# Optimization experiments

Measured on AMD Instinct MI355X. Metric: run time of the kernel, lower is better.

Reference implementation:

```python
import jax, jax.numpy as jnp
import numpy as np

N = 100000
E = 640000
D_IN = 128
D_OUT = 128


def setup_inputs() -> dict:
    key = jax.random.key(0)
    k1, k2, k3, k4, k5 = jax.random.split(key, 5)
    x = jax.random.normal(k1, (N, D_IN), dtype=jnp.float32)
    edge_index = jax.random.randint(k2, (2, E), 0, N, dtype=jnp.int64)
    edge_weight = jax.random.uniform(k3, (E,), dtype=jnp.float32)
    W_rel = jax.random.normal(k4, (D_OUT, D_IN), dtype=jnp.float32) / np.sqrt(D_IN)
    W_root = jax.random.normal(k5, (D_OUT, D_IN), dtype=jnp.float32) / np.sqrt(D_IN)
    b = jnp.zeros((D_OUT,), dtype=jnp.float32)
    return {"x": x, "edge_index": edge_index, "edge_weight": edge_weight,
            "W_rel": W_rel, "W_root": W_root, "b": b}


def reference(x, edge_index, edge_weight, W_rel, W_root, b):
    # PyG GraphConv: out_i = W_rel @ (sum_{j -> i} w_ij * x_j) + W_root @ x_i + b
    src = edge_index[0]  # message source (x_j)
    dst = edge_index[1]  # aggregation target
    msg = x[src] * edge_weight[:, None]          # [E, D_IN] gather + scale
    agg = jax.ops.segment_sum(msg, dst, num_segments=x.shape[0])  # [N, D_IN]
    out = agg @ W_rel.T + x @ W_root.T + b       # [N, D_OUT]
    return out
```

## Files before the change

kernel.cpp:

```cpp
#include <hip/hip_runtime.h>
#include <hip/hip_fp16.h>

#define NN 100000
#define EE 640000
#define D 128
#define NBINS NN
#define SCAN_NBLK 98

#define WS_CNT      0
#define WS_OFFS     100000
#define WS_BSUM     200000
#define WS_SW       200192
#define WS_WF       1480192
#define WS_XH       1496576
#define WS_INTS_TOP 7896576

#define WS_WCONV    1480192
#define WS_INTS_MID 1512960

#define PREP_XB 3125
#define PREP_WB 128
#define PREP_HB 2500

typedef __attribute__((ext_vector_type(8))) short    short8v;
typedef __attribute__((ext_vector_type(8))) _Float16 half8v;
typedef __attribute__((ext_vector_type(4))) float    floatx4;
struct __align__(8) half4t { __half2 a, b; };

__device__ inline void split_bf16(float f, short& h, short& l) {
    unsigned u  = __float_as_uint(f);
    unsigned hb = u & 0xFFFF0000u;
    h = (short)(u >> 16);
    float fl = f - __uint_as_float(hb);
    l = (short)(__float_as_uint(fl) >> 16);
}

__global__ __launch_bounds__(256) void scatter_kernel(
    const float* __restrict__ x, const int* __restrict__ ei,
    const float* __restrict__ ew, float* agg)
{
    int gid = blockIdx.x * 256 + threadIdx.x;
    int e = gid >> 7, f = gid & 127;
    if (e >= EE) return;
    float v = x[ei[e] * D + f] * ew[e];
    unsafeAtomicAdd(&agg[ei[EE + e] * D + f], v);
}

__global__ __launch_bounds__(256) void zero_cnt_kernel(int* __restrict__ cnt)
{
    int i = blockIdx.x * 256 + threadIdx.x;
    if (i < NBINS) cnt[i] = 0;
}

__global__ __launch_bounds__(256) void prep_kernel(
    const float* __restrict__ x, const float* __restrict__ Wrel,
    const float* __restrict__ Wroot, const int* __restrict__ ei,
    short* __restrict__ xh, short* __restrict__ Wf, int* __restrict__ cnt)
{
    const int b = blockIdx.x;
    if (b < PREP_XB) {
        const int base = b * 4096 + threadIdx.x * 4;
        float4 v[4];
        #pragma unroll
        for (int u = 0; u < 4; u++)
            v[u] = *(const float4*)&x[base + u * 1024];
        #pragma unroll
        for (int u = 0; u < 4; u++) {
            short4 h;
            h.x = (short)__half_as_ushort(__float2half(v[u].x));
            h.y = (short)__half_as_ushort(__float2half(v[u].y));
            h.z = (short)__half_as_ushort(__float2half(v[u].z));
            h.w = (short)__half_as_ushort(__float2half(v[u].w));
            *(short4*)&xh[base + u * 1024] = h;
        }
    } else if (b < PREP_XB + PREP_WB) {
        int i = (b - PREP_XB) * 256 + threadIdx.x;
        int c = i >> 8, k = i & 255;
        float f = (k < 128) ? Wrel[c * 128 + k] : Wroot[c * 128 + (k - 128)];
        Wf[i] = (short)__half_as_ushort(__float2half(f));
    } else {
        int e = (b - PREP_XB - PREP_WB) * 256 + threadIdx.x;
        if (e < EE) atomicAdd(&cnt[ei[EE + e]], 1);
    }
}

__global__ __launch_bounds__(256) void hist_kernel(
    const int* __restrict__ ei, int* __restrict__ cnt)
{
    int e = blockIdx.x * 256 + threadIdx.x;
    if (e < EE) atomicAdd(&cnt[ei[EE + e]], 1);
}

__global__ __launch_bounds__(256) void wconv_kernel(
    const float* __restrict__ Wrel, const float* __restrict__ Wroot,
    short* __restrict__ Wb)
{
    int i = blockIdx.x * 256 + threadIdx.x;
    int c = i >> 8, k = i & 255;
    float f = (k < 128) ? Wrel[c * 128 + k] : Wroot[c * 128 + (k - 128)];
    short h, l;
    split_bf16(f, h, l);
    Wb[i] = h;
    Wb[32768 + i] = l;
}

__global__ __launch_bounds__(256) void scanA_kernel(
    const int* __restrict__ cnt, int* __restrict__ offs, int* __restrict__ bsum)
{
    __shared__ int tsum[256];
    const int tid = threadIdx.x;
    const int base = blockIdx.x * 1024 + tid * 4;
    int v[4], s = 0;
    #pragma unroll
    for (int i = 0; i < 4; i++) {
        int idx = base + i;
        v[i] = (idx < NBINS) ? cnt[idx] : 0;
        s += v[i];
    }
    tsum[tid] = s;
    __syncthreads();
    for (int off = 1; off < 256; off <<= 1) {
        int t = (tid >= off) ? tsum[tid - off] : 0;
        __syncthreads();
        tsum[tid] += t;
        __syncthreads();
    }
    int run = tsum[tid] - s;
    #pragma unroll
    for (int i = 0; i < 4; i++) {
        int idx = base + i;
        if (idx < NBINS) offs[idx] = run;
        run += v[i];
    }
    if (tid == 255) bsum[blockIdx.x] = tsum[255];
}

__global__ __launch_bounds__(256) void scanC_kernel(
    int* __restrict__ offs, const int* __restrict__ bsum)
{
    __shared__ int s[128];
    const int tid = threadIdx.x;
    if (tid < 128) s[tid] = (tid < SCAN_NBLK) ? bsum[tid] : 0;
    __syncthreads();
    for (int off = 1; off < 128; off <<= 1) {
        int t = 0;
        if (tid < 128 && tid >= off) t = s[tid - off];
        __syncthreads();
        if (tid < 128) s[tid] += t;
        __syncthreads();
    }
    const int add = (blockIdx.x == 0) ? 0 : s[blockIdx.x - 1];
    const int base = blockIdx.x * 1024 + tid * 4;
    #pragma unroll
    for (int i = 0; i < 4; i++) {
        int idx = base + i;
        if (idx < NBINS) offs[idx] += add;
    }
}

__global__ __launch_bounds__(256) void build_kernel(
    const int* __restrict__ ei, const float* __restrict__ ew,
    int* __restrict__ offs, int2* __restrict__ sw)
{
    int e = blockIdx.x * 256 + threadIdx.x;
    if (e >= EE) return;
    int dst = ei[EE + e];
    int p = atomicAdd(&offs[dst], 1);
    sw[p] = make_int2(ei[e], __float_as_int(ew[e]));
}

__global__ __launch_bounds__(256) void aggregate_h_kernel(
    const short* __restrict__ xh, const int* __restrict__ offs,
    const int2* __restrict__ sw, float* __restrict__ out)
{
    const int node = blockIdx.x * 8 + (threadIdx.x >> 5);
    const int fl   = threadIdx.x & 31;
    if (node >= NN) return;
    const int beg = (node == 0) ? 0 : offs[node - 1];
    const int end = offs[node];
    const half4t* xp = (const half4t*)xh;

    float4 a0 = make_float4(0.f, 0.f, 0.f, 0.f);
    float4 a1 = make_float4(0.f, 0.f, 0.f, 0.f);
    int j = beg;
    for (; j + 3 < end; j += 4) {
        int2 s0 = sw[j], s1 = sw[j + 1], s2 = sw[j + 2], s3 = sw[j + 3];
        half4t v0 = xp[(size_t)s0.x * 32 + fl];
        half4t v1 = xp[(size_t)s1.x * 32 + fl];
        half4t v2 = xp[(size_t)s2.x * 32 + fl];
        half4t v3 = xp[(size_t)s3.x * 32 + fl];
        float w0 = __int_as_float(s0.y), w1 = __int_as_float(s1.y);
        float w2 = __int_as_float(s2.y), w3 = __int_as_float(s3.y);
        float2 l0 = __half22float2(v0.a), h0 = __half22float2(v0.b);
        float2 l1 = __half22float2(v1.a), h1 = __half22float2(v1.b);
        float2 l2 = __half22float2(v2.a), h2 = __half22float2(v2.b);
        float2 l3 = __half22float2(v3.a), h3 = __half22float2(v3.b);
        a0.x += w0 * l0.x; a0.y += w0 * l0.y; a0.z += w0 * h0.x; a0.w += w0 * h0.y;
        a1.x += w1 * l1.x; a1.y += w1 * l1.y; a1.z += w1 * h1.x; a1.w += w1 * h1.y;
        a0.x += w2 * l2.x; a0.y += w2 * l2.y; a0.z += w2 * h2.x; a0.w += w2 * h2.y;
        a1.x += w3 * l3.x; a1.y += w3 * l3.y; a1.z += w3 * h3.x; a1.w += w3 * h3.y;
    }
    for (; j + 1 < end; j += 2) {
        int2 s0 = sw[j], s1 = sw[j + 1];
        half4t v0 = xp[(size_t)s0.x * 32 + fl];
        half4t v1 = xp[(size_t)s1.x * 32 + fl];
        float w0 = __int_as_float(s0.y), w1 = __int_as_float(s1.y);
        float2 l0 = __half22float2(v0.a), h0 = __half22float2(v0.b);
        float2 l1 = __half22float2(v1.a), h1 = __half22float2(v1.b);
        a0.x += w0 * l0.x; a0.y += w0 * l0.y; a0.z += w0 * h0.x; a0.w += w0 * h0.y;
        a1.x += w1 * l1.x; a1.y += w1 * l1.y; a1.z += w1 * h1.x; a1.w += w1 * h1.y;
    }
    if (j < end) {
        int2 s0 = sw[j];
        half4t v0 = xp[(size_t)s0.x * 32 + fl];
        float w0 = __int_as_float(s0.y);
        float2 l0 = __half22float2(v0.a), h0 = __half22float2(v0.b);
        a0.x += w0 * l0.x; a0.y += w0 * l0.y; a0.z += w0 * h0.x; a0.w += w0 * h0.y;
    }
    float4 r = make_float4(a0.x + a1.x, a0.y + a1.y, a0.z + a1.z, a0.w + a1.w);
    half4t o;
    o.a = __floats2half2_rn(r.x, r.y);
    o.b = __floats2half2_rn(r.z, r.w);
    half4t* op = (half4t*)((char*)out + (size_t)node * 512 + 256);
    op[fl] = o;
}

__global__ __launch_bounds__(256) void aggregate_kernel(
    const float* __restrict__ x, const int* __restrict__ offs,
    const int2* __restrict__ sw, float* __restrict__ out)
{
    const int node = blockIdx.x * 8 + (threadIdx.x >> 5);
    const int fl   = threadIdx.x & 31;
    if (node >= NN) return;
    const int beg = (node == 0) ? 0 : offs[node - 1];
    const int end = offs[node];
    const float4* x4 = (const float4*)x;

    float4 a0 = make_float4(0.f, 0.f, 0.f, 0.f);
    float4 a1 = make_float4(0.f, 0.f, 0.f, 0.f);
    int j = beg;
    for (; j + 1 < end; j += 2) {
        int2 s0 = sw[j];
        int2 s1 = sw[j + 1];
        float4 v0 = x4[(size_t)s0.x * 32 + fl];
        float4 v1 = x4[(size_t)s1.x * 32 + fl];
        float w0 = __int_as_float(s0.y), w1 = __int_as_float(s1.y);
        a0.x += w0 * v0.x; a0.y += w0 * v0.y; a0.z += w0 * v0.z; a0.w += w0 * v0.w;
        a1.x += w1 * v1.x; a1.y += w1 * v1.y; a1.z += w1 * v1.z; a1.w += w1 * v1.w;
    }
    if (j < end) {
        int2 s0 = sw[j];
        float4 v0 = x4[(size_t)s0.x * 32 + fl];
        float w0 = __int_as_float(s0.y);
        a0.x += w0 * v0.x; a0.y += w0 * v0.y; a0.z += w0 * v0.z; a0.w += w0 * v0.w;
    }
    float4 r = make_float4(a0.x + a1.x, a0.y + a1.y, a0.z + a1.z, a0.w + a1.w);
    ((float4*)out)[(size_t)node * 32 + fl] = r;
}

__global__ __launch_bounds__(256) void mfma_f16_kernel(
    const short* __restrict__ xh, const short* __restrict__ Wf,
    const float* __restrict__ bias, float* __restrict__ out)
{
    __shared__ short lds[2 * 128 * 64];
    short* At = lds;
    short* Wt = lds + 8192;

    const int tid  = threadIdx.x;
    const int lane = tid & 63;
    const int wave = tid >> 6;
    const int row0 = blockIdx.x * 128;
    const int frow = lane & 15;

    floatx4 acc[2][8];
    #pragma unroll
    for (int nf = 0; nf < 8; nf++) {
        float b = bias[nf * 16 + frow];
        #pragma unroll
        for (int mf = 0; mf < 2; mf++) acc[mf][nf] = (floatx4){b, b, b, b};
    }

    const short* aggh = (const short*)out;

    for (int kc = 0; kc < 4; kc++) {
        __syncthreads();
        #pragma unroll
        for (int i = 0; i < 4; i++) {
            int e = (i * 256 + tid) * 8;
            int r = e >> 6, k = e & 63;
            int rg = row0 + r;
            short8v v = (short8v)0;
            if (rg < NN) {
                if (kc < 2) v = *(const short8v*)&aggh[(size_t)rg * 256 + 128 + kc * 64 + k];
                else        v = *(const short8v*)&xh[(size_t)rg * 128 + (kc - 2) * 64 + k];
            }
            int sidx = r * 64 + (((k >> 3) ^ (r & 7)) << 3);
            *(short8v*)&At[sidx] = v;
        }
        #pragma unroll
        for (int i = 0; i < 4; i++) {
            int e = (i * 256 + tid) * 8;
            int c = e >> 6, k = e & 63;
            int sidx = c * 64 + (((k >> 3) ^ (c & 7)) << 3);
            *(short8v*)&Wt[sidx] = *(const short8v*)&Wf[c * 256 + kc * 64 + k];
        }
        __syncthreads();

        const int arow = wave * 32;
        #pragma unroll
        for (int kf = 0; kf < 2; kf++) {
            const int kblk = kf * 4 + (lane >> 4);
            half8v a[2];
            #pragma unroll
            for (int mf = 0; mf < 2; mf++) {
                int r = arow + mf * 16 + frow;
                int idx = r * 64 + ((kblk ^ (r & 7)) << 3);
                a[mf] = *(const half8v*)&At[idx];
            }
            #pragma unroll
            for (int nf = 0; nf < 8; nf++) {
                int cc = nf * 16 + frow;
                int idx = cc * 64 + ((kblk ^ (cc & 7)) << 3);
                half8v b = *(const half8v*)&Wt[idx];
                #pragma unroll
                for (int mf = 0; mf < 2; mf++)
                    acc[mf][nf] = __builtin_amdgcn_mfma_f32_16x16x32_f16(a[mf], b, acc[mf][nf], 0, 0, 0);
            }
        }
    }

    const int orow = row0 + wave * 32;
    #pragma unroll
    for (int mf = 0; mf < 2; mf++) {
        #pragma unroll
        for (int j = 0; j < 4; j++) {
            int r = orow + mf * 16 + (lane >> 4) * 4 + j;
            if (r < NN) {
                #pragma unroll
                for (int nf = 0; nf < 8; nf++)
                    out[(size_t)r * D + nf * 16 + (lane & 15)] = acc[mf][nf][j];
            }
        }
    }
}

__global__ __launch_bounds__(256) void mfma_gemm_kernel(
    const float* __restrict__ x, const short* __restrict__ Wb,
    const float* __restrict__ bias, float* __restrict__ out)
{
    __shared__ short lds[4 * 128 * 64];
    short* Ah = lds;
    short* Al = lds + 8192;
    short* Wh = lds + 16384;
    short* Wl = lds + 24576;

    const int tid  = threadIdx.x;
    const int lane = tid & 63;
    const int wave = tid >> 6;
    const int row0 = blockIdx.x * 128;
    const int frow = lane & 15;
    const int fk   = (lane >> 4) * 8;

    floatx4 acc[2][8];
    #pragma unroll
    for (int nf = 0; nf < 8; nf++) {
        float b = bias[nf * 16 + frow];
        #pragma unroll
        for (int mf = 0; mf < 2; mf++) acc[mf][nf] = (floatx4){b, b, b, b};
    }

    for (int kc = 0; kc < 4; kc++) {
        const float* A = (kc < 2) ? out : x;
        const int kcol = (kc & 1) * 64;
        __syncthreads();
        #pragma unroll
        for (int i = 0; i < 8; i++) {
            int e = (i * 256 + tid) * 4;
            int r = e >> 6, k = e & 63;
            int rg = row0 + r;
            float4 v = (rg < NN) ? *(const float4*)&A[(size_t)rg * D + kcol + k]
                                 : make_float4(0.f, 0.f, 0.f, 0.f);
            short4 h, l;
            split_bf16(v.x, h.x, l.x);
            split_bf16(v.y, h.y, l.y);
            split_bf16(v.z, h.z, l.z);
            split_bf16(v.w, h.w, l.w);
            int sidx = r * 64 + (((k >> 3) ^ (r & 7)) << 3) + (k & 7);
            *(short4*)&Ah[sidx] = h;
            *(short4*)&Al[sidx] = l;
        }
        #pragma unroll
        for (int i = 0; i < 4; i++) {
            int e = (i * 256 + tid) * 8;
            int c = e >> 6, k = e & 63;
            int sidx = c * 64 + (((k >> 3) ^ (c & 7)) << 3);
            int g = c * 256 + kc * 64 + k;
// ... 64 lines not shown
    for (int phase = 0; phase < 2; phase++) {
        const float* A = phase ? x : out;
        const float* W = (phase ? Wroot : Wrel) + wid * 16 * D;
        __syncthreads();
        #pragma unroll
        for (int i = 0; i < 16; i++) {
            int e = i * 512 + tid;
            int r = e >> 7, k = e & 127;
            int rg = row0 + r;
            AtT[k][r] = (rg < NN) ? A[rg * D + k] : 0.0f;
        }
        __syncthreads();
        for (int k4 = 0; k4 < 32; k4++) {
            float a0 = AtT[k4 * 4 + 0][lane];
            float a1 = AtT[k4 * 4 + 1][lane];
            float a2 = AtT[k4 * 4 + 2][lane];
            float a3 = AtT[k4 * 4 + 3][lane];
            #pragma unroll
            for (int c = 0; c < 16; c++) {
                const float* wp = W + c * D + k4 * 4;
                acc[c] += a0 * wp[0] + a1 * wp[1] + a2 * wp[2] + a3 * wp[3];
            }
        }
    }
    __syncthreads();
    #pragma unroll
    for (int c = 0; c < 16; c++)
        AtT[wid * 16 + c][lane] = acc[c];
    __syncthreads();
    #pragma unroll
    for (int i = 0; i < 16; i++) {
        int e = i * 512 + tid;
        int r = e >> 7, col = e & 127;
        int rg = row0 + r;
        if (rg < NN) out[rg * D + col] = AtT[col][r];
    }
}

extern "C" void kernel_launch(void* const* d_in, const int* in_sizes, int n_in,
                              void* d_out, int out_size, void* d_ws, size_t ws_size,
                              hipStream_t stream) {
    const float* x     = (const float*)d_in[0];
    const int*   ei    = (const int*)  d_in[1];
    const float* ew    = (const float*)d_in[2];
    const float* Wrel  = (const float*)d_in[3];
    const float* Wroot = (const float*)d_in[4];
    const float* bias  = (const float*)d_in[5];
    float*       out   = (float*)d_out;

    const int eb = (EE + 255) / 256;

    if (ws_size >= (size_t)WS_INTS_TOP * sizeof(int)) {
        int* w = (int*)d_ws;
        int*   cnt  = w + WS_CNT;
        int*   offs = w + WS_OFFS;
        int*   bsum = w + WS_BSUM;
        int2*  sw   = (int2*)(w + WS_SW);
        short* Wf   = (short*)(w + WS_WF);
        short* xh   = (short*)(w + WS_XH);

        zero_cnt_kernel<<<(NBINS + 255) / 256, 256, 0, stream>>>(cnt);
        prep_kernel<<<PREP_XB + PREP_WB + PREP_HB, 256, 0, stream>>>(
            x, Wrel, Wroot, ei, xh, Wf, cnt);
        scanA_kernel<<<SCAN_NBLK, 256, 0, stream>>>(cnt, offs, bsum);
        scanC_kernel<<<SCAN_NBLK, 256, 0, stream>>>(offs, bsum);
        build_kernel<<<eb, 256, 0, stream>>>(ei, ew, offs, sw);
        aggregate_h_kernel<<<NN / 8, 256, 0, stream>>>(xh, offs, sw, out);
        mfma_f16_kernel<<<(NN + 127) / 128, 256, 0, stream>>>(xh, Wf, bias, out);
    } else if (ws_size >= (size_t)WS_INTS_MID * sizeof(int)) {
        int* w = (int*)d_ws;
        int*   cnt  = w + WS_CNT;
        int*   offs = w + WS_OFFS;
        int*   bsum = w + WS_BSUM;
        int2*  sw   = (int2*)(w + WS_SW);
        short* Wb   = (short*)(w + WS_WCONV);

        zero_cnt_kernel<<<(NBINS + 255) / 256, 256, 0, stream>>>(cnt);
        wconv_kernel<<<128, 256, 0, stream>>>(Wrel, Wroot, Wb);
        hist_kernel <<<eb, 256, 0, stream>>>(ei, cnt);
        scanA_kernel<<<SCAN_NBLK, 256, 0, stream>>>(cnt, offs, bsum);
        scanC_kernel<<<SCAN_NBLK, 256, 0, stream>>>(offs, bsum);
        build_kernel<<<eb, 256, 0, stream>>>(ei, ew, offs, sw);
        aggregate_kernel<<<NN / 8, 256, 0, stream>>>(x, offs, sw, out);
        mfma_gemm_kernel<<<(NN + 127) / 128, 256, 0, stream>>>(x, Wb, bias, out);
    } else {
        hipMemsetAsync(out, 0, (size_t)NN * D * sizeof(float), stream);
        scatter_kernel<<<(EE * 128) / 256, 256, 0, stream>>>(x, ei, ew, out);
        gemm_kernel<<<(NN + 63) / 64, 512, 0, stream>>>(x, Wrel, Wroot, bias, out);
    }
}
```

Before: 138.9 us.

## Split degree histogram into 8 partitions and record edge slots to skip build atomics

The histogram now spreads counts over 8 partitioned copies chosen by block index, which cuts atomic contention on popular destination bins. Each edge records its returned slot, so the build step computes its output position directly instead of issuing a second atomic. The scan handles all 8 partitions and produces CSR offsets with an explicit end entry. In exchange the histogram array is 8x larger, scan traffic rises, and a 640K-entry slot array is written and read back. It also requires a larger workspace to take the fast path.

```diff
diff --git a/kernel.cpp b/kernel.cpp
--- a/kernel.cpp
+++ b/kernel.cpp
@@ -7,14 +7,22 @@
 #define NBINS NN
 #define SCAN_NBLK 98
 
+#define CSTRIDE 100352
+#define OSTRIDE 100032
+
+#define WS_CNT8     0
+#define WS_OFFSX    802816
+#define WS_BSUM     1603072
+#define WS_ESLOT    1603200
+#define WS_SW       2243200
+#define WS_WF       3523200
+#define WS_XH       3539584
+#define WS_INTS_TOP 9939584
+
 #define WS_CNT      0
 #define WS_OFFS     100000
-#define WS_BSUM     200000
-#define WS_SW       200192
-#define WS_WF       1480192
-#define WS_XH       1496576
-#define WS_INTS_TOP 7896576
-
+#define WS_BSUMM    200000
+#define WS_SWM      200192
 #define WS_WCONV    1480192
 #define WS_INTS_MID 1512960
 
@@ -46,6 +54,12 @@
     unsafeAtomicAdd(&agg[ei[EE + e] * D + f], v);
 }
 
+__global__ __launch_bounds__(256) void zero8_kernel(int* __restrict__ cnt8)
+{
+    int i = blockIdx.x * 256 + threadIdx.x;
+    if (i < 8 * CSTRIDE) cnt8[i] = 0;
+}
+
 __global__ __launch_bounds__(256) void zero_cnt_kernel(int* __restrict__ cnt)
 {
     int i = blockIdx.x * 256 + threadIdx.x;
@@ -55,7 +69,8 @@
 __global__ __launch_bounds__(256) void prep_kernel(
     const float* __restrict__ x, const float* __restrict__ Wrel,
     const float* __restrict__ Wroot, const int* __restrict__ ei,
-    short* __restrict__ xh, short* __restrict__ Wf, int* __restrict__ cnt)
+    short* __restrict__ xh, short* __restrict__ Wf,
+    int* __restrict__ cnt8, int* __restrict__ eslot)
 {
     const int b = blockIdx.x;
     if (b < PREP_XB) {
@@ -80,42 +95,35 @@
         Wf[i] = (short)__half_as_ushort(__float2half(f));
     } else {
         int e = (b - PREP_XB - PREP_WB) * 256 + threadIdx.x;
-        if (e < EE) atomicAdd(&cnt[ei[EE + e]], 1);
-    }
-}
-
-__global__ __launch_bounds__(256) void hist_kernel(
-    const int* __restrict__ ei, int* __restrict__ cnt)
-{
-    int e = blockIdx.x * 256 + threadIdx.x;
-    if (e < EE) atomicAdd(&cnt[ei[EE + e]], 1);
-}
-
-__global__ __launch_bounds__(256) void wconv_kernel(
-    const float* __restrict__ Wrel, const float* __restrict__ Wroot,
-    short* __restrict__ Wb)
-{
-    int i = blockIdx.x * 256 + threadIdx.x;
-    int c = i >> 8, k = i & 255;
-    float f = (k < 128) ? Wrel[c * 128 + k] : Wroot[c * 128 + (k - 128)];
-    short h, l;
-    split_bf16(f, h, l);
-    Wb[i] = h;
-    Wb[32768 + i] = l;
-}
-
-__global__ __launch_bounds__(256) void scanA_kernel(
-    const int* __restrict__ cnt, int* __restrict__ offs, int* __restrict__ bsum)
+        if (e < EE) {
+            int dst  = ei[EE + e];
+            int cp   = b & 7;
+            int slot = atomicAdd(&cnt8[cp * CSTRIDE + dst], 1);
+            eslot[e] = (slot << 3) | cp;
+        }
+    }
+}
+
+__global__ __launch_bounds__(256) void scanA8_kernel(
+    const int* __restrict__ cnt8, int* __restrict__ offsx, int* __restrict__ bsum)
 {
     __shared__ int tsum[256];
     const int tid = threadIdx.x;
     const int base = blockIdx.x * 1024 + tid * 4;
-    int v[4], s = 0;
+    int v[4], pc[8][4];
+    int s = 0;
     #pragma unroll
     for (int i = 0; i < 4; i++) {
-        int idx = base + i;
-        v[i] = (idx < NBINS) ? cnt[idx] : 0;
-        s += v[i];
+        int bin = base + i;
+        int run = 0;
+        #pragma unroll
+        for (int cp = 0; cp < 8; cp++) {
+            int cv = (bin < NBINS) ? cnt8[cp * CSTRIDE + bin] : 0;
+            pc[cp][i] = run;
+            run += cv;
+        }
+        v[i] = run;
+        s += run;
     }
     tsum[tid] = s;
     __syncthreads();
@@ -128,15 +136,19 @@
     int run = tsum[tid] - s;
     #pragma unroll
     for (int i = 0; i < 4; i++) {
-        int idx = base + i;
-        if (idx < NBINS) offs[idx] = run;
+        int bin = base + i;
+        if (bin < NBINS) {
+            #pragma unroll
+            for (int cp = 0; cp < 8; cp++)
+                offsx[cp * OSTRIDE + bin] = run + pc[cp][i];
+        }
         run += v[i];
     }
     if (tid == 255) bsum[blockIdx.x] = tsum[255];
 }
 
-__global__ __launch_bounds__(256) void scanC_kernel(
-    int* __restrict__ offs, const int* __restrict__ bsum)
+__global__ __launch_bounds__(256) void scanC8_kernel(
+    int* __restrict__ offsx, const int* __restrict__ bsum)
 {
     __shared__ int s[128];
     const int tid = threadIdx.x;
@@ -153,31 +165,38 @@
     const int base = blockIdx.x * 1024 + tid * 4;
     #pragma unroll
     for (int i = 0; i < 4; i++) {
-        int idx = base + i;
-        if (idx < NBINS) offs[idx] += add;
-    }
+        int bin = base + i;
+        if (bin < NBINS) {
+            #pragma unroll
+            for (int cp = 0; cp < 8; cp++)
+                offsx[cp * OSTRIDE + bin] += add;
+        }
+    }
+    if (blockIdx.x == 0 && tid == 0) offsx[NN] = EE;
 }
 
 __global__ __launch_bounds__(256) void build_kernel(
     const int* __restrict__ ei, const float* __restrict__ ew,
-    int* __restrict__ offs, int2* __restrict__ sw)
+    const int* __restrict__ offsx, const int* __restrict__ eslot,
+    int2* __restrict__ sw)
 {
     int e = blockIdx.x * 256 + threadIdx.x;
     if (e >= EE) return;
     int dst = ei[EE + e];
-    int p = atomicAdd(&offs[dst], 1);
+    int es  = eslot[e];
+    int p   = offsx[(es & 7) * OSTRIDE + dst] + (es >> 3);
     sw[p] = make_int2(ei[e], __float_as_int(ew[e]));
 }
 
 __global__ __launch_bounds__(256) void aggregate_h_kernel(
-    const short* __restrict__ xh, const int* __restrict__ offs,
+    const short* __restrict__ xh, const int* __restrict__ offsx,
     const int2* __restrict__ sw, float* __restrict__ out)
 {
     const int node = blockIdx.x * 8 + (threadIdx.x >> 5);
     const int fl   = threadIdx.x & 31;
     if (node >= NN) return;
-    const int beg = (node == 0) ? 0 : offs[node - 1];
-    const int end = offs[node];
+    const int beg = offsx[node];
+    const int end = offsx[node + 1];
     const half4t* xp = (const half4t*)xh;
 
     float4 a0 = make_float4(0.f, 0.f, 0.f, 0.f);
@@ -225,6 +244,177 @@
     op[fl] = o;
 }
 
+__global__ __launch_bounds__(256) void mfma_f16_kernel(
+    const short* __restrict__ xh, const short* __restrict__ Wf,
+    const float* __restrict__ bias, float* __restrict__ out)
+{
+    __shared__ short lds[2 * 128 * 64];
+    short* At = lds;
+    short* Wt = lds + 8192;
+
+    const int tid  = threadIdx.x;
+    const int lane = tid & 63;
+    const int wave = tid >> 6;
+    const int row0 = blockIdx.x * 128;
+    const int frow = lane & 15;
+
+    floatx4 acc[2][8];
+    #pragma unroll
+    for (int nf = 0; nf < 8; nf++) {
+        float b = bias[nf * 16 + frow];
+        #pragma unroll
+        for (int mf = 0; mf < 2; mf++) acc[mf][nf] = (floatx4){b, b, b, b};
+    }
+
+    const short* aggh = (const short*)out;
+
+    for (int kc = 0; kc < 4; kc++) {
+        __syncthreads();
+        #pragma unroll
+        for (int i = 0; i < 4; i++) {
+            int e = (i * 256 + tid) * 8;
+            int r = e >> 6, k = e & 63;
+            int rg = row0 + r;
+            short8v v = (short8v)0;
+            if (rg < NN) {
+                if (kc < 2) v = *(const short8v*)&aggh[(size_t)rg * 256 + 128 + kc * 64 + k];
+                else        v = *(const short8v*)&xh[(size_t)rg * 128 + (kc - 2) * 64 + k];
+            }
+            int sidx = r * 64 + (((k >> 3) ^ (r & 7)) << 3);
+            *(short8v*)&At[sidx] = v;
+        }
+        #pragma unroll
+        for (int i = 0; i < 4; i++) {
+            int e = (i * 256 + tid) * 8;
+            int c = e >> 6, k = e & 63;
+            int sidx = c * 64 + (((k >> 3) ^ (c & 7)) << 3);
+            *(short8v*)&Wt[sidx] = *(const short8v*)&Wf[c * 256 + kc * 64 + k];
+        }
+        __syncthreads();
+
+        const int arow = wave * 32;
+        #pragma unroll
+        for (int kf = 0; kf < 2; kf++) {
+            const int kblk = kf * 4 + (lane >> 4);
+            half8v a[2];
+            #pragma unroll
+            for (int mf = 0; mf < 2; mf++) {
+                int r = arow + mf * 16 + frow;
+                int idx = r * 64 + ((kblk ^ (r & 7)) << 3);
+                a[mf] = *(const half8v*)&At[idx];
+            }
+            #pragma unroll
+            for (int nf = 0; nf < 8; nf++) {
+                int cc = nf * 16 + frow;
+                int idx = cc * 64 + ((kblk ^ (cc & 7)) << 3);
+                half8v b = *(const half8v*)&Wt[idx];
+                #pragma unroll
+                for (int mf = 0; mf < 2; mf++)
+                    acc[mf][nf] = __builtin_amdgcn_mfma_f32_16x16x32_f16(a[mf], b, acc[mf][nf], 0, 0, 0);
+            }
+        }
+    }
+
+    const int orow = row0 + wave * 32;
+    #pragma unroll
+    for (int mf = 0; mf < 2; mf++) {
+        #pragma unroll
+        for (int j = 0; j < 4; j++) {
+            int r = orow + mf * 16 + (lane >> 4) * 4 + j;
+            if (r < NN) {
+                #pragma unroll
+                for (int nf = 0; nf < 8; nf++)
+                    out[(size_t)r * D + nf * 16 + (lane & 15)] = acc[mf][nf][j];
+            }
+        }
+    }
+}
+
+__global__ __launch_bounds__(256) void hist_kernel(
+    const int* __restrict__ ei, int* __restrict__ cnt)
+{
+    int e = blockIdx.x * 256 + threadIdx.x;
+    if (e < EE) atomicAdd(&cnt[ei[EE + e]], 1);
+}
+
+__global__ __launch_bounds__(256) void wconv_kernel(
+    const float* __restrict__ Wrel, const float* __restrict__ Wroot,
+    short* __restrict__ Wb)
+{
+    int i = blockIdx.x * 256 + threadIdx.x;
+    int c = i >> 8, k = i & 255;
+    float f = (k < 128) ? Wrel[c * 128 + k] : Wroot[c * 128 + (k - 128)];
+    short h, l;
+    split_bf16(f, h, l);
+    Wb[i] = h;
+    Wb[32768 + i] = l;
+}
+
+__global__ __launch_bounds__(256) void scanA_kernel(
+    const int* __restrict__ cnt, int* __restrict__ offs, int* __restrict__ bsum)
+{
+    __shared__ int tsum[256];
+    const int tid = threadIdx.x;
+    const int base = blockIdx.x * 1024 + tid * 4;
+    int v[4], s = 0;
+    #pragma unroll
+    for (int i = 0; i < 4; i++) {
+        int idx = base + i;
+        v[i] = (idx < NBINS) ? cnt[idx] : 0;
+        s += v[i];
+    }
+    tsum[tid] = s;
+    __syncthreads();
+    for (int off = 1; off < 256; off <<= 1) {
+        int t = (tid >= off) ? tsum[tid - off] : 0;
+        __syncthreads();
+        tsum[tid] += t;
+        __syncthreads();
+    }
+    int run = tsum[tid] - s;
+    #pragma unroll
+    for (int i = 0; i < 4; i++) {
+        int idx = base + i;
+        if (idx < NBINS) offs[idx] = run;
+        run += v[i];
+    }
+    if (tid == 255) bsum[blockIdx.x] = tsum[255];
+}
+
+__global__ __launch_bounds__(256) void scanC_kernel(
+    int* __restrict__ offs, const int* __restrict__ bsum)
+{
+    __shared__ int s[128];
+    const int tid = threadIdx.x;
+    if (tid < 128) s[tid] = (tid < SCAN_NBLK) ? bsum[tid] : 0;
+    __syncthreads();
+    for (int off = 1; off < 128; off <<= 1) {
+        int t = 0;
+        if (tid < 128 && tid >= off) t = s[tid - off];
+        __syncthreads();
+        if (tid < 128) s[tid] += t;
+        __syncthreads();
+    }
+    const int add = (blockIdx.x == 0) ? 0 : s[blockIdx.x - 1];
+    const int base = blockIdx.x * 1024 + tid * 4;
+    #pragma unroll
+    for (int i = 0; i < 4; i++) {
+        int idx = base + i;
+        if (idx < NBINS) offs[idx] += add;
+    }
+}
+
+__global__ __launch_bounds__(256) void buildM_kernel(
+    const int* __restrict__ ei, const float* __restrict__ ew,
+    int* __restrict__ offs, int2* __restrict__ sw)
+{
+    int e = blockIdx.x * 256 + threadIdx.x;
+    if (e >= EE) return;
+    int dst = ei[EE + e];
+    int p = atomicAdd(&offs[dst], 1);
+    sw[p] = make_int2(ei[e], __float_as_int(ew[e]));
+}
+
 __global__ __launch_bounds__(256) void aggregate_kernel(
     const float* __restrict__ x, const int* __restrict__ offs,
     const int2* __restrict__ sw, float* __restrict__ out)
@@ -256,92 +446,6 @@
     }
     float4 r = make_float4(a0.x + a1.x, a0.y + a1.y, a0.z + a1.z, a0.w + a1.w);
     ((float4*)out)[(size_t)node * 32 + fl] = r;
-}
-
-__global__ __launch_bounds__(256) void mfma_f16_kernel(
-    const short* __restrict__ xh, const short* __restrict__ Wf,
-    const float* __restrict__ bias, float* __restrict__ out)
-{
-    __shared__ short lds[2 * 128 * 64];
-    short* At = lds;
-    short* Wt = lds + 8192;
-
-    const int tid  = threadIdx.x;
-    const int lane = tid & 63;
-    const int wave = tid >> 6;
-    const int row0 = blockIdx.x * 128;
-    const int frow = lane & 15;
-
-    floatx4 acc[2][8];
-    #pragma unroll
-    for (int nf = 0; nf < 8; nf++) {
-        float b = bias[nf * 16 + frow];
-        #pragma unroll
-        for (int mf = 0; mf < 2; mf++) acc[mf][nf] = (floatx4){b, b, b, b};
-    }
-
-    const short* aggh = (const short*)out;
-
-    for (int kc = 0; kc < 4; kc++) {
-        __syncthreads();
-        #pragma unroll
-        for (int i = 0; i < 4; i++) {
-            int e = (i * 256 + tid) * 8;
-            int r = e >> 6, k = e & 63;
-            int rg = row0 + r;
-            short8v v = (short8v)0;
-            if (rg < NN) {
-                if (kc < 2) v = *(const short8v*)&aggh[(size_t)rg * 256 + 128 + kc * 64 + k];
-                else        v = *(const short8v*)&xh[(size_t)rg * 128 + (kc - 2) * 64 + k];
-            }
-            int sidx = r * 64 + (((k >> 3) ^ (r & 7)) << 3);
-            *(short8v*)&At[sidx] = v;
-        }
-        #pragma unroll
-        for (int i = 0; i < 4; i++) {
-            int e = (i * 256 + tid) * 8;
-            int c = e >> 6, k = e & 63;
-            int sidx = c * 64 + (((k >> 3) ^ (c & 7)) << 3);
-            *(short8v*)&Wt[sidx] = *(const short8v*)&Wf[c * 256 + kc * 64 + k];
-        }
-        __syncthreads();
-
-        const int arow = wave * 32;
-        #pragma unroll
-        for (int kf = 0; kf < 2; kf++) {
-            const int kblk = kf * 4 + (lane >> 4);
-            half8v a[2];
-            #pragma unroll
-            for (int mf = 0; mf < 2; mf++) {
-                int r = arow + mf * 16 + frow;
-                int idx = r * 64 + ((kblk ^ (r & 7)) << 3);
-                a[mf] = *(const half8v*)&At[idx];
-            }
-            #pragma unroll
-            for (int nf = 0; nf < 8; nf++) {
-                int cc = nf * 16 + frow;
-                int idx = cc * 64 + ((kblk ^ (cc & 7)) << 3);
-                half8v b = *(const half8v*)&Wt[idx];
-                #pragma unroll
-                for (int mf = 0; mf < 2; mf++)
-                    acc[mf][nf] = __builtin_amdgcn_mfma_f32_16x16x32_f16(a[mf], b, acc[mf][nf], 0, 0, 0);
-            }
-        }
-    }
-
-    const int orow = row0 + wave * 32;
-    #pragma unroll
-    for (int mf = 0; mf < 2; mf++) {
-        #pragma unroll
-        for (int j = 0; j < 4; j++) {
-            int r = orow + mf * 16 + (lane >> 4) * 4 + j;
-            if (r < NN) {
-                #pragma unroll
-                for (int nf = 0; nf < 8; nf++)
-                    out[(size_t)r * D + nf * 16 + (lane & 15)] = acc[mf][nf][j];
-            }
-        }
-    }
 }
 
 __global__ __launch_bounds__(256) void mfma_gemm_kernel(
@@ -512,27 +616,28 @@
 
     if (ws_size >= (size_t)WS_INTS_TOP * sizeof(int)) {
         int* w = (int*)d_ws;
-        int*   cnt  = w + WS_CNT;
-        int*   offs = w + WS_OFFS;
-        int*   bsum = w + WS_BSUM;
-        int2*  sw   = (int2*)(w + WS_SW);
-        short* Wf   = (short*)(w + WS_WF);
-        short* xh   = (short*)(w + WS_XH);
-
-        zero_cnt_kernel<<<(NBINS + 255) / 256, 256, 0, stream>>>(cnt);
+        int*   cnt8  = w + WS_CNT8;
+        int*   offsx = w + WS_OFFSX;
+        int*   bsum  = w + WS_BSUM;
+        int*   eslot = w + WS_ESLOT;
+        int2*  sw    = (int2*)(w + WS_SW);
+        short* Wf    = (short*)(w + WS_WF);
+        short* xh    = (short*)(w + WS_XH);
+
+        zero8_kernel<<<(8 * CSTRIDE) / 256, 256, 0, stream>>>(cnt8);
         prep_kernel<<<PREP_XB + PREP_WB + PREP_HB, 256, 0, stream>>>(
-            x, Wrel, Wroot, ei, xh, Wf, cnt);
-        scanA_kernel<<<SCAN_NBLK, 256, 0, stream>>>(cnt, offs, bsum);
-        scanC_kernel<<<SCAN_NBLK, 256, 0, stream>>>(offs, bsum);
-        build_kernel<<<eb, 256, 0, stream>>>(ei, ew, offs, sw);
-        aggregate_h_kernel<<<NN / 8, 256, 0, stream>>>(xh, offs, sw, out);
+            x, Wrel, Wroot, ei, xh, Wf, cnt8, eslot);
+        scanA8_kernel<<<SCAN_NBLK, 256, 0, stream>>>(cnt8, offsx, bsum);
+        scanC8_kernel<<<SCAN_NBLK, 256, 0, stream>>>(offsx, bsum);
+        build_kernel<<<eb, 256, 0, stream>>>(ei, ew, offsx, eslot, sw);
+        aggregate_h_kernel<<<NN / 8, 256, 0, stream>>>(xh, offsx, sw, out);
         mfma_f16_kernel<<<(NN + 127) / 128, 256, 0, stream>>>(xh, Wf, bias, out);
     } else if (ws_size >= (size_t)WS_INTS_MID * sizeof(int)) {
         int* w = (int*)d_ws;
         int*   cnt  = w + WS_CNT;
         int*   offs = w + WS_OFFS;
-        int*   bsum = w + WS_BSUM;
-        int2*  sw   = (int2*)(w + WS_SW);
+        int*   bsum = w + WS_BSUMM;
+        int2*  sw   = (int2*)(w + WS_SWM);
         short* Wb   = (short*)(w + WS_WCONV);
 
         zero_cnt_kernel<<<(NBINS + 255) / 256, 256, 0, stream>>>(cnt);
@@ -540,7 +645,7 @@
         hist_kernel <<<eb, 256, 0, stream>>>(ei, cnt);
         scanA_kernel<<<SCAN_NBLK, 256, 0, stream>>>(cnt, offs, bsum);
         scanC_kernel<<<SCAN_NBLK, 256, 0, stream>>>(offs, bsum);
-        build_kernel<<<eb, 256, 0, stream>>>(ei, ew, offs, sw);
+        buildM_kernel<<<eb, 256, 0, stream>>>(ei, ew, offs, sw);
         aggregate_kernel<<<NN / 8, 256, 0, stream>>>(x, offs, sw, out);
         mfma_gemm_kernel<<<(NN + 127) / 128, 256, 0, stream>>>(x, Wb, bias, out);
     } else {
```

After: 130.4 us. 1.07x faster.

## Replace global-atomic CSR build with two-level bucketed counting sort

Applied to the files above, without the earlier changes.

Swaps the per-node global atomic histogram, the scan and the atomic scatter build for a two-level counting sort. Edges are first binned into 64-node buckets with per-block shared-memory histograms, a column scan and a bucket scan, then each bucket is sorted locally in LDS. The aggregated fp16 rows now go to a separate workspace buffer rather than being staged inside the output array, so the GEMM reads two clean inputs. The aim is to cut global atomic contention and random writes, at the cost of an extra edge pass, a larger workspace and a single-block scan kernel.

```diff
diff --git a/kernel.cpp b/kernel.cpp
--- a/kernel.cpp
+++ b/kernel.cpp
@@ -7,20 +7,31 @@
 #define NBINS NN
 #define SCAN_NBLK 98
 
-#define WS_CNT      0
-#define WS_OFFS     100000
-#define WS_BSUM     200000
-#define WS_SW       200192
-#define WS_WF       1480192
-#define WS_XH       1496576
-#define WS_INTS_TOP 7896576
-
+#define BKT 1563
+#define EBLK 256
+#define EPB 2500
+
+#define WS_LCNT     0
+#define WS_TOT      400128
+#define WS_BOFFS    401728
+#define WS_OFFS     403328
+#define WS_SW       503360
+#define WS_SW2      1783360
+#define WS_WF       3063360
+#define WS_XH       3079744
+#define WS_AGGD     9479744
+#define WS_INTS_TOP 15879744
+
+#define WS_CNTM     0
+#define WS_OFFSM    100000
+#define WS_BSUMM    200000
+#define WS_SWM      200192
 #define WS_WCONV    1480192
 #define WS_INTS_MID 1512960
 
 #define PREP_XB 3125
 #define PREP_WB 128
-#define PREP_HB 2500
+#define PREP_AB EBLK
 
 typedef __attribute__((ext_vector_type(8))) short    short8v;
 typedef __attribute__((ext_vector_type(8))) _Float16 half8v;
@@ -46,17 +57,12 @@
     unsafeAtomicAdd(&agg[ei[EE + e] * D + f], v);
 }
 
-__global__ __launch_bounds__(256) void zero_cnt_kernel(int* __restrict__ cnt)
-{
-    int i = blockIdx.x * 256 + threadIdx.x;
-    if (i < NBINS) cnt[i] = 0;
-}
-
-__global__ __launch_bounds__(256) void prep_kernel(
+__global__ __launch_bounds__(256) void prepA_kernel(
     const float* __restrict__ x, const float* __restrict__ Wrel,
     const float* __restrict__ Wroot, const int* __restrict__ ei,
-    short* __restrict__ xh, short* __restrict__ Wf, int* __restrict__ cnt)
-{
+    short* __restrict__ xh, short* __restrict__ Wf, int* __restrict__ lcnt)
+{
+    __shared__ int h[BKT];
     const int b = blockIdx.x;
     if (b < PREP_XB) {
         const int base = b * 4096 + threadIdx.x * 4;
@@ -66,12 +72,12 @@
             v[u] = *(const float4*)&x[base + u * 1024];
         #pragma unroll
         for (int u = 0; u < 4; u++) {
-            short4 h;
-            h.x = (short)__half_as_ushort(__float2half(v[u].x));
-            h.y = (short)__half_as_ushort(__float2half(v[u].y));
-            h.z = (short)__half_as_ushort(__float2half(v[u].z));
-            h.w = (short)__half_as_ushort(__float2half(v[u].w));
-            *(short4*)&xh[base + u * 1024] = h;
+            short4 hh;
+            hh.x = (short)__half_as_ushort(__float2half(v[u].x));
+            hh.y = (short)__half_as_ushort(__float2half(v[u].y));
+            hh.z = (short)__half_as_ushort(__float2half(v[u].z));
+            hh.w = (short)__half_as_ushort(__float2half(v[u].w));
+            *(short4*)&xh[base + u * 1024] = hh;
         }
     } else if (b < PREP_XB + PREP_WB) {
         int i = (b - PREP_XB) * 256 + threadIdx.x;
@@ -79,112 +85,136 @@
         float f = (k < 128) ? Wrel[c * 128 + k] : Wroot[c * 128 + (k - 128)];
         Wf[i] = (short)__half_as_ushort(__float2half(f));
     } else {
-        int e = (b - PREP_XB - PREP_WB) * 256 + threadIdx.x;
-        if (e < EE) atomicAdd(&cnt[ei[EE + e]], 1);
-    }
-}
-
-__global__ __launch_bounds__(256) void hist_kernel(
-    const int* __restrict__ ei, int* __restrict__ cnt)
-{
-    int e = blockIdx.x * 256 + threadIdx.x;
-    if (e < EE) atomicAdd(&cnt[ei[EE + e]], 1);
-}
-
-__global__ __launch_bounds__(256) void wconv_kernel(
-    const float* __restrict__ Wrel, const float* __restrict__ Wroot,
-    short* __restrict__ Wb)
-{
-    int i = blockIdx.x * 256 + threadIdx.x;
-    int c = i >> 8, k = i & 255;
-    float f = (k < 128) ? Wrel[c * 128 + k] : Wroot[c * 128 + (k - 128)];
-    short h, l;
-    split_bf16(f, h, l);
-    Wb[i] = h;
-    Wb[32768 + i] = l;
-}
-
-__global__ __launch_bounds__(256) void scanA_kernel(
-    const int* __restrict__ cnt, int* __restrict__ offs, int* __restrict__ bsum)
-{
-    __shared__ int tsum[256];
-    const int tid = threadIdx.x;
-    const int base = blockIdx.x * 1024 + tid * 4;
-    int v[4], s = 0;
-    #pragma unroll
-    for (int i = 0; i < 4; i++) {
-        int idx = base + i;
-        v[i] = (idx < NBINS) ? cnt[idx] : 0;
-        s += v[i];
-    }
-    tsum[tid] = s;
-    __syncthreads();
-    for (int off = 1; off < 256; off <<= 1) {
-        int t = (tid >= off) ? tsum[tid - off] : 0;
-        __syncthreads();
-        tsum[tid] += t;
-        __syncthreads();
-    }
-    int run = tsum[tid] - s;
-    #pragma unroll
-    for (int i = 0; i < 4; i++) {
-        int idx = base + i;
-        if (idx < NBINS) offs[idx] = run;
-        run += v[i];
-    }
-    if (tid == 255) bsum[blockIdx.x] = tsum[255];
-}
-
-__global__ __launch_bounds__(256) void scanC_kernel(
-    int* __restrict__ offs, const int* __restrict__ bsum)
-{
-    __shared__ int s[128];
-    const int tid = threadIdx.x;
-    if (tid < 128) s[tid] = (tid < SCAN_NBLK) ? bsum[tid] : 0;
-    __syncthreads();
-    for (int off = 1; off < 128; off <<= 1) {
+        const int eb = b - PREP_XB - PREP_WB;
+        for (int i = threadIdx.x; i < BKT; i += 256) h[i] = 0;
+        __syncthreads();
+        const int e0 = eb * EPB, e1 = e0 + EPB;
+        for (int e = e0 + threadIdx.x; e < e1; e += 256)
+            atomicAdd(&h[ei[EE + e] >> 6], 1);
+        __syncthreads();
+        for (int i = threadIdx.x; i < BKT; i += 256)
+            lcnt[eb * BKT + i] = h[i];
+    }
+}
+
+__global__ __launch_bounds__(256) void colscan_kernel(
+    int* __restrict__ lcnt, int* __restrict__ tot)
+{
+    int t = blockIdx.x * 256 + threadIdx.x;
+    if (t >= BKT) return;
+    int run = 0;
+    for (int b = 0; b < EBLK; b++) {
+        int v = lcnt[b * BKT + t];
+        lcnt[b * BKT + t] = run;
+        run += v;
+    }
+    tot[t] = run;
+}
+
+__global__ __launch_bounds__(256) void scanT_kernel(
+    const int* __restrict__ tot, int* __restrict__ boffs)
+{
+    __shared__ int s[256];
+    __shared__ int carry;
+    if (threadIdx.x == 0) carry = 0;
+    __syncthreads();
+    for (int c = 0; c < 7; c++) {
+        int idx = c * 256 + threadIdx.x;
+        int v = (idx < BKT) ? tot[idx] : 0;
+        s[threadIdx.x] = v;
+        __syncthreads();
+        for (int off = 1; off < 256; off <<= 1) {
+            int t = (threadIdx.x >= off) ? s[threadIdx.x - off] : 0;
+            __syncthreads();
+            s[threadIdx.x] += t;
+            __syncthreads();
+        }
+        if (idx < BKT) boffs[idx] = carry + s[threadIdx.x] - v;
+        __syncthreads();
+        if (threadIdx.x == 0) carry += s[255];
+        __syncthreads();
+    }
+    if (threadIdx.x == 0) boffs[BKT] = EE;
+}
+
+__global__ __launch_bounds__(256) void passB_kernel(
+    const int* __restrict__ ei, const float* __restrict__ ew,
+    const int* __restrict__ lcnt, const int* __restrict__ boffs,
+    int2* __restrict__ sw)
+{
+    __shared__ int base2[BKT];
+    __shared__ int cur[BKT];
+    const int eb = blockIdx.x;
+    for (int i = threadIdx.x; i < BKT; i += 256) {
+        base2[i] = boffs[i] + lcnt[eb * BKT + i];
+        cur[i] = 0;
+    }
+    __syncthreads();
+    const int e0 = eb * EPB, e1 = e0 + EPB;
+    for (int e = e0 + threadIdx.x; e < e1; e += 256) {
+        int src = ei[e];
+        int dst = ei[EE + e];
+        int bkt = dst >> 6;
+        int r = atomicAdd(&cur[bkt], 1);
+        sw[base2[bkt] + r] = make_int2(src | ((dst & 63) << 17),
+                                       __float_as_int(ew[e]));
+    }
+}
+
+__global__ __launch_bounds__(256) void passC_kernel(
+    const int2* __restrict__ sw, const int* __restrict__ boffs,
+    int2* __restrict__ sw2, int* __restrict__ offs)
+{
+    __shared__ int cnt[64], nb[64], cur[64];
+    __shared__ int segbeg, segend;
+    const int bkt = blockIdx.x;
+    if (threadIdx.x == 0) { segbeg = boffs[bkt]; segend = boffs[bkt + 1]; }
+    if (threadIdx.x < 64) { cnt[threadIdx.x] = 0; cur[threadIdx.x] = 0; }
+    __syncthreads();
+    for (int j = segbeg + threadIdx.x; j < segend; j += 256)
+        atomicAdd(&cnt[(sw[j].x >> 17) & 63], 1);
+    __syncthreads();
+    if (threadIdx.x < 64) nb[threadIdx.x] = cnt[threadIdx.x];
+    __syncthreads();
+    for (int off = 1; off < 64; off <<= 1) {
         int t = 0;
-        if (tid < 128 && tid >= off) t = s[tid - off];
-        __syncthreads();
-        if (tid < 128) s[tid] += t;
-        __syncthreads();
-    }
-    const int add = (blockIdx.x == 0) ? 0 : s[blockIdx.x - 1];
-    const int base = blockIdx.x * 1024 + tid * 4;
-    #pragma unroll
-    for (int i = 0; i < 4; i++) {
-        int idx = base + i;
-        if (idx < NBINS) offs[idx] += add;
-    }
-}
-
-__global__ __launch_bounds__(256) void build_kernel(
-    const int* __restrict__ ei, const float* __restrict__ ew,
-    int* __restrict__ offs, int2* __restrict__ sw)
-{
-    int e = blockIdx.x * 256 + threadIdx.x;
-    if (e >= EE) return;
-    int dst = ei[EE + e];
-    int p = atomicAdd(&offs[dst], 1);
-    sw[p] = make_int2(ei[e], __float_as_int(ew[e]));
+        if (threadIdx.x < 64 && threadIdx.x >= off) t = nb[threadIdx.x - off];
+        __syncthreads();
+        if (threadIdx.x < 64) nb[threadIdx.x] += t;
+        __syncthreads();
+    }
+    if (threadIdx.x < 64) {
+        int b = segbeg + nb[threadIdx.x] - cnt[threadIdx.x];
+        nb[threadIdx.x] = b;
+        int node = bkt * 64 + threadIdx.x;
+        if (node < NN) offs[node] = b;
+    }
+    __syncthreads();
+    for (int j = segbeg + threadIdx.x; j < segend; j += 256) {
+        int2 v = sw[j];
+        int n = (v.x >> 17) & 63;
+        int r = atomicAdd(&cur[n], 1);
+        sw2[nb[n] + r] = make_int2(v.x & 0x1FFFF, v.y);
+    }
+    if (bkt == 0 && threadIdx.x == 0) offs[NN] = EE;
 }
 
 __global__ __launch_bounds__(256) void aggregate_h_kernel(
     const short* __restrict__ xh, const int* __restrict__ offs,
-    const int2* __restrict__ sw, float* __restrict__ out)
+    const int2* __restrict__ sw2, short* __restrict__ aggd)
 {
     const int node = blockIdx.x * 8 + (threadIdx.x >> 5);
     const int fl   = threadIdx.x & 31;
     if (node >= NN) return;
-    const int beg = (node == 0) ? 0 : offs[node - 1];
-    const int end = offs[node];
+    const int beg = offs[node];
+    const int end = offs[node + 1];
     const half4t* xp = (const half4t*)xh;
 
     float4 a0 = make_float4(0.f, 0.f, 0.f, 0.f);
     float4 a1 = make_float4(0.f, 0.f, 0.f, 0.f);
     int j = beg;
     for (; j + 3 < end; j += 4) {
-        int2 s0 = sw[j], s1 = sw[j + 1], s2 = sw[j + 2], s3 = sw[j + 3];
+        int2 s0 = sw2[j], s1 = sw2[j + 1], s2 = sw2[j + 2], s3 = sw2[j + 3];
         half4t v0 = xp[(size_t)s0.x * 32 + fl];
         half4t v1 = xp[(size_t)s1.x * 32 + fl];
         half4t v2 = xp[(size_t)s2.x * 32 + fl];
@@ -201,7 +231,7 @@
         a1.x += w3 * l3.x; a1.y += w3 * l3.y; a1.z += w3 * h3.x; a1.w += w3 * h3.y;
     }
     for (; j + 1 < end; j += 2) {
-        int2 s0 = sw[j], s1 = sw[j + 1];
+        int2 s0 = sw2[j], s1 = sw2[j + 1];
         half4t v0 = xp[(size_t)s0.x * 32 + fl];
         half4t v1 = xp[(size_t)s1.x * 32 + fl];
         float w0 = __int_as_float(s0.y), w1 = __int_as_float(s1.y);
@@ -211,7 +241,7 @@
         a1.x += w1 * l1.x; a1.y += w1 * l1.y; a1.z += w1 * h1.x; a1.w += w1 * h1.y;
     }
     if (j < end) {
-        int2 s0 = sw[j];
+        int2 s0 = sw2[j];
         half4t v0 = xp[(size_t)s0.x * 32 + fl];
         float w0 = __int_as_float(s0.y);
         float2 l0 = __half22float2(v0.a), h0 = __half22float2(v0.b);
@@ -221,46 +251,13 @@
     half4t o;
     o.a = __floats2half2_rn(r.x, r.y);
     o.b = __floats2half2_rn(r.z, r.w);
-    half4t* op = (half4t*)((char*)out + (size_t)node * 512 + 256);
-    op[fl] = o;
-}
-
-__global__ __launch_bounds__(256) void aggregate_kernel(
-    const float* __restrict__ x, const int* __restrict__ offs,
-    const int2* __restrict__ sw, float* __restrict__ out)
-{
-    const int node = blockIdx.x * 8 + (threadIdx.x >> 5);
-    const int fl   = threadIdx.x & 31;
-    if (node >= NN) return;
-    const int beg = (node == 0) ? 0 : offs[node - 1];
-    const int end = offs[node];
-    const float4* x4 = (const float4*)x;
-
-    float4 a0 = make_float4(0.f, 0.f, 0.f, 0.f);
-    float4 a1 = make_float4(0.f, 0.f, 0.f, 0.f);
-    int j = beg;
-    for (; j + 1 < end; j += 2) {
-        int2 s0 = sw[j];
-        int2 s1 = sw[j + 1];
-        float4 v0 = x4[(size_t)s0.x * 32 + fl];
-        float4 v1 = x4[(size_t)s1.x * 32 + fl];
-        float w0 = __int_as_float(s0.y), w1 = __int_as_float(s1.y);
-        a0.x += w0 * v0.x; a0.y += w0 * v0.y; a0.z += w0 * v0.z; a0.w += w0 * v0.w;
-        a1.x += w1 * v1.x; a1.y += w1 * v1.y; a1.z += w1 * v1.z; a1.w += w1 * v1.w;
-    }
-    if (j < end) {
-        int2 s0 = sw[j];
-        float4 v0 = x4[(size_t)s0.x * 32 + fl];
-        float w0 = __int_as_float(s0.y);
-        a0.x += w0 * v0.x; a0.y += w0 * v0.y; a0.z += w0 * v0.z; a0.w += w0 * v0.w;
-    }
-    float4 r = make_float4(a0.x + a1.x, a0.y + a1.y, a0.z + a1.z, a0.w + a1.w);
-    ((float4*)out)[(size_t)node * 32 + fl] = r;
+    ((half4t*)aggd)[(size_t)node * 32 + fl] = o;
 }
 
 __global__ __launch_bounds__(256) void mfma_f16_kernel(
-    const short* __restrict__ xh, const short* __restrict__ Wf,
-    const float* __restrict__ bias, float* __restrict__ out)
+    const short* __restrict__ xh, const short* __restrict__ aggd,
+    const short* __restrict__ Wf, const float* __restrict__ bias,
+    float* __restrict__ out)
 {
     __shared__ short lds[2 * 128 * 64];
     short* At = lds;
@@ -280,9 +277,9 @@
         for (int mf = 0; mf < 2; mf++) acc[mf][nf] = (floatx4){b, b, b, b};
     }
 
-    const short* aggh = (const short*)out;
-
     for (int kc = 0; kc < 4; kc++) {
+        const short* A = (kc < 2) ? aggd : xh;
+        const int kcol = (kc & 1) * 64;
         __syncthreads();
         #pragma unroll
         for (int i = 0; i < 4; i++) {
@@ -290,10 +287,7 @@
             int r = e >> 6, k = e & 63;
             int rg = row0 + r;
             short8v v = (short8v)0;
-            if (rg < NN) {
-                if (kc < 2) v = *(const short8v*)&aggh[(size_t)rg * 256 + 128 + kc * 64 + k];
-                else        v = *(const short8v*)&xh[(size_t)rg * 128 + (kc - 2) * 64 + k];
-            }
+            if (rg < NN) v = *(const short8v*)&A[(size_t)rg * 128 + kcol + k];
             int sidx = r * 64 + (((k >> 3) ^ (r & 7)) << 3);
             *(short8v*)&At[sidx] = v;
         }
@@ -342,6 +336,130 @@
             }
         }
     }
+}
+
+__global__ __launch_bounds__(256) void zero_cnt_kernel(int* __restrict__ cnt)
+{
+    int i = blockIdx.x * 256 + threadIdx.x;
+    if (i < NBINS) cnt[i] = 0;
+}
+
+__global__ __launch_bounds__(256) void hist_kernel(
+    const int* __restrict__ ei, int* __restrict__ cnt)
+{
+    int e = blockIdx.x * 256 + threadIdx.x;
+    if (e < EE) atomicAdd(&cnt[ei[EE + e]], 1);
+}
+
+__global__ __launch_bounds__(256) void wconv_kernel(
+    const float* __restrict__ Wrel, const float* __restrict__ Wroot,
+    short* __restrict__ Wb)
+{
+    int i = blockIdx.x * 256 + threadIdx.x;
+    int c = i >> 8, k = i & 255;
+    float f = (k < 128) ? Wrel[c * 128 + k] : Wroot[c * 128 + (k - 128)];
+    short h, l;
+    split_bf16(f, h, l);
+    Wb[i] = h;
+    Wb[32768 + i] = l;
+}
+
+__global__ __launch_bounds__(256) void scanA_kernel(
+    const int* __restrict__ cnt, int* __restrict__ offs, int* __restrict__ bsum)
+{
+    __shared__ int tsum[256];
+    const int tid = threadIdx.x;
+    const int base = blockIdx.x * 1024 + tid * 4;
+    int v[4], s = 0;
+    #pragma unroll
+    for (int i = 0; i < 4; i++) {
+        int idx = base + i;
+        v[i] = (idx < NBINS) ? cnt[idx] : 0;
+        s += v[i];
+    }
+    tsum[tid] = s;
+    __syncthreads();
+    for (int off = 1; off < 256; off <<= 1) {
+        int t = (tid >= off) ? tsum[tid - off] : 0;
+        __syncthreads();
+        tsum[tid] += t;
+        __syncthreads();
+    }
+    int run = tsum[tid] - s;
+    #pragma unroll
+    for (int i = 0; i < 4; i++) {
+        int idx = base + i;
+        if (idx < NBINS) offs[idx] = run;
+        run += v[i];
+    }
+    if (tid == 255) bsum[blockIdx.x] = tsum[255];
+}
+
+__global__ __launch_bounds__(256) void scanC_kernel(
+    int* __restrict__ offs, const int* __restrict__ bsum)
+{
+    __shared__ int s[128];
+    const int tid = threadIdx.x;
+    if (tid < 128) s[tid] = (tid < SCAN_NBLK) ? bsum[tid] : 0;
+    __syncthreads();
+    for (int off = 1; off < 128; off <<= 1) {
+        int t = 0;
+        if (tid < 128 && tid >= off) t = s[tid - off];
+        __syncthreads();
+        if (tid < 128) s[tid] += t;
+        __syncthreads();
+    }
+    const int add = (blockIdx.x == 0) ? 0 : s[blockIdx.x - 1];
+    const int base = blockIdx.x * 1024 + tid * 4;
+    #pragma unroll
+    for (int i = 0; i < 4; i++) {
+        int idx = base + i;
+        if (idx < NBINS) offs[idx] += add;
+    }
+}
+
+__global__ __launch_bounds__(256) void buildM_kernel(
+    const int* __restrict__ ei, const float* __restrict__ ew,
+    int* __restrict__ offs, int2* __restrict__ sw)
+{
+    int e = blockIdx.x * 256 + threadIdx.x;
+    if (e >= EE) return;
+    int dst = ei[EE + e];
+    int p = atomicAdd(&offs[dst], 1);
+    sw[p] = make_int2(ei[e], __float_as_int(ew[e]));
+}
+
+__global__ __launch_bounds__(256) void aggregate_kernel(
+    const float* __restrict__ x, const int* __restrict__ offs,
+    const int2* __restrict__ sw, float* __restrict__ out)
+{
+    const int node = blockIdx.x * 8 + (threadIdx.x >> 5);
+    const int fl   = threadIdx.x & 31;
+    if (node >= NN) return;
+    const int beg = (node == 0) ? 0 : offs[node - 1];
+    const int end = offs[node];
+    const float4* x4 = (const float4*)x;
+
+    float4 a0 = make_float4(0.f, 0.f, 0.f, 0.f);
+    float4 a1 = make_float4(0.f, 0.f, 0.f, 0.f);
+    int j = beg;
+    for (; j + 1 < end; j += 2) {
+        int2 s0 = sw[j];
+        int2 s1 = sw[j + 1];
+        float4 v0 = x4[(size_t)s0.x * 32 + fl];
+        float4 v1 = x4[(size_t)s1.x * 32 + fl];
+        float w0 = __int_as_float(s0.y), w1 = __int_as_float(s1.y);
+        a0.x += w0 * v0.x; a0.y += w0 * v0.y; a0.z += w0 * v0.z; a0.w += w0 * v0.w;
+        a1.x += w1 * v1.x; a1.y += w1 * v1.y; a1.z += w1 * v1.z; a1.w += w1 * v1.w;
+    }
+    if (j < end) {
+        int2 s0 = sw[j];
+        float4 v0 = x4[(size_t)s0.x * 32 + fl];
+        float w0 = __int_as_float(s0.y);
+        a0.x += w0 * v0.x; a0.y += w0 * v0.y; a0.z += w0 * v0.z; a0.w += w0 * v0.w;
+    }
+    float4 r = make_float4(a0.x + a1.x, a0.y + a1.y, a0.z + a1.z, a0.w + a1.w);
+    ((float4*)out)[(size_t)node * 32 + fl] = r;
 }
 
 __global__ __launch_bounds__(256) void mfma_gemm_kernel(
@@ -512,27 +630,30 @@
 
     if (ws_size >= (size_t)WS_INTS_TOP * sizeof(int)) {
         int* w = (int*)d_ws;
-        int*   cnt  = w + WS_CNT;
-        int*   offs = w + WS_OFFS;
-        int*   bsum = w + WS_BSUM;
-        int2*  sw   = (int2*)(w + WS_SW);
-        short* Wf   = (short*)(w + WS_WF);
-        short* xh   = (short*)(w + WS_XH);
-
-        zero_cnt_kernel<<<(NBINS + 255) / 256, 256, 0, stream>>>(cnt);
-        prep_kernel<<<PREP_XB + PREP_WB + PREP_HB, 256, 0, stream>>>(
-            x, Wrel, Wroot, ei, xh, Wf, cnt);
-        scanA_kernel<<<SCAN_NBLK, 256, 0, stream>>>(cnt, offs, bsum);
-        scanC_kernel<<<SCAN_NBLK, 256, 0, stream>>>(offs, bsum);
-        build_kernel<<<eb, 256, 0, stream>>>(ei, ew, offs, sw);
-        aggregate_h_kernel<<<NN / 8, 256, 0, stream>>>(xh, offs, sw, out);
-        mfma_f16_kernel<<<(NN + 127) / 128, 256, 0, stream>>>(xh, Wf, bias, out);
+        int*   lcnt  = w + WS_LCNT;
+        int*   tot   = w + WS_TOT;
+        int*   boffs = w + WS_BOFFS;
+        int*   offs  = w + WS_OFFS;
+        int2*  sw    = (int2*)(w + WS_SW);
+        int2*  sw2   = (int2*)(w + WS_SW2);
+        short* Wf    = (short*)(w + WS_WF);
+        short* xh    = (short*)(w + WS_XH);
+        short* aggd  = (short*)(w + WS_AGGD);
+
+        prepA_kernel<<<PREP_XB + PREP_WB + PREP_AB, 256, 0, stream>>>(
+            x, Wrel, Wroot, ei, xh, Wf, lcnt);
+        colscan_kernel<<<(BKT + 255) / 256, 256, 0, stream>>>(lcnt, tot);
+        scanT_kernel<<<1, 256, 0, stream>>>(tot, boffs);
+        passB_kernel<<<EBLK, 256, 0, stream>>>(ei, ew, lcnt, boffs, sw);
+        passC_kernel<<<BKT, 256, 0, stream>>>(sw, boffs, sw2, offs);
+        aggregate_h_kernel<<<NN / 8, 256, 0, stream>>>(xh, offs, sw2, aggd);
+        mfma_f16_kernel<<<(NN + 127) / 128, 256, 0, stream>>>(xh, aggd, Wf, bias, out);
     } else if (ws_size >= (size_t)WS_INTS_MID * sizeof(int)) {
         int* w = (int*)d_ws;
-        int*   cnt  = w + WS_CNT;
-        int*   offs = w + WS_OFFS;
-        int*   bsum = w + WS_BSUM;
-        int2*  sw   = (int2*)(w + WS_SW);
+        int*   cnt  = w + WS_CNTM;
+        int*   offs = w + WS_OFFSM;
+        int*   bsum = w + WS_BSUMM;
+        int2*  sw   = (int2*)(w + WS_SWM);
         short* Wb   = (short*)(w + WS_WCONV);
 
         zero_cnt_kernel<<<(NBINS + 255) / 256, 256, 0, stream>>>(cnt);
@@ -540,7 +661,7 @@
         hist_kernel <<<eb, 256, 0, stream>>>(ei, cnt);
         scanA_kernel<<<SCAN_NBLK, 256, 0, stream>>>(cnt, offs, bsum);
         scanC_kernel<<<SCAN_NBLK, 256, 0, stream>>>(offs, bsum);
-        build_kernel<<<eb, 256, 0, stream>>>(ei, ew, offs, sw);
+        buildM_kernel<<<eb, 256, 0, stream>>>(ei, ew, offs, sw);
         aggregate_kernel<<<NN / 8, 256, 0, stream>>>(x, offs, sw, out);
         mfma_gemm_kernel<<<(NN + 127) / 128, 256, 0, stream>>>(x, Wb, bias, out);
     } else {
```

Result: faster. 116.7 us, median of 2 (-16.0%).
